# Performance work log

Measured on AMD Instinct MI355X. Metric: run time of the kernel, lower is better.

The kernel has to match this reference:

```python
import jax, jax.numpy as jnp
import numpy as np

EPS = 1e-5
L = 19        # number of semantic labels (fc_mu0..fc_mu18)
S = 512       # style_length


def conv3x3(x, w, b):
    # x: [B,C,H,W], w: [O,I,3,3] (torch OIHW), b: [O]
    y = jax.lax.conv_general_dilated(
        x, w, window_strides=(1, 1), padding='SAME',
        dimension_numbers=('NCHW', 'OIHW', 'NCHW'))
    return y + b[None, :, None, None]


def setup_inputs() -> dict:
    key = jax.random.key(0)
    ks = jax.random.split(key, 20)
    B, FIN, H, W = 4, 128, 256, 256
    inp = {
        'x': jax.random.normal(ks[0], (B, FIN, H, W), jnp.float32),
        'labels': jax.random.randint(ks[1], (B, H, W), 0, L),
        'noise': jax.random.normal(ks[2], (B, W, H, 1), jnp.float32),
        'style_codes': jax.random.normal(ks[3], (B, L, S), jnp.float32),
        # params
        'noise_var': 0.02 * jax.random.normal(ks[4], (FIN,), jnp.float32),
        'w_sh': 0.02 * jax.random.normal(ks[5], (128, L, 3, 3), jnp.float32),
        'b_sh': jnp.zeros((128,), jnp.float32),
        'w_g': 0.02 * jax.random.normal(ks[6], (FIN, 128, 3, 3), jnp.float32),
        'b_g': jnp.zeros((FIN,), jnp.float32),
        'w_b': 0.02 * jax.random.normal(ks[7], (FIN, 128, 3, 3), jnp.float32),
        'b_b': jnp.zeros((FIN,), jnp.float32),
        'Wfc': 0.02 * jax.random.normal(ks[8], (L, S, S), jnp.float32),  # [label, out, in]
        'bfc': jnp.zeros((L, S), jnp.float32),
        'w_cg': 0.02 * jax.random.normal(ks[9], (FIN, S, 3, 3), jnp.float32),
        'b_cg': jnp.zeros((FIN,), jnp.float32),
        'w_cb': 0.02 * jax.random.normal(ks[10], (FIN, S, 3, 3), jnp.float32),
        'b_cb': jnp.zeros((FIN,), jnp.float32),
        'g_blend': jnp.zeros((1,), jnp.float32),
        'b_blend': jnp.zeros((1,), jnp.float32),
    }
    return inp


def reference(x, labels, noise, style_codes, noise_var, w_sh, b_sh, w_g, b_g,
              w_b, b_b, Wfc, bfc, w_cg, b_cg, w_cb, b_cb, g_blend, b_blend):
    B, FIN, H, W = x.shape
    # added_noise: randn([B,W,H,1]) * noise_var[FIN] then transpose(1,3) -> [B,FIN,H,W]
    added = jnp.transpose(noise * noise_var, (0, 3, 2, 1))
    xn = x + added
    # param-free BatchNorm2d (training-mode batch stats, biased var)
    mean = jnp.mean(xn, axis=(0, 2, 3), keepdims=True)
    var = jnp.mean(jnp.square(xn - mean), axis=(0, 2, 3), keepdims=True)
    normalized = (xn - mean) / jnp.sqrt(var + EPS)

    # one-hot segmap [B,L,H,W]; interpolation to x's size is identity here
    seg = jnp.transpose(jax.nn.one_hot(labels, L, dtype=x.dtype), (0, 3, 1, 2))

    # per-label style FC: mu[b,j,:] = relu(fc_mu_j(style_codes[b,j]))
    mu = jax.nn.relu(jnp.einsum('bjd,jod->bjo', style_codes, Wfc) + bfc)  # [B,L,S]
    # masked_scatter with one-hot masks == per-pixel gather of the label's style code
    middle = mu[jnp.arange(B)[:, None, None], labels]        # [B,H,W,S]
    middle = jnp.transpose(middle, (0, 3, 1, 2))              # [B,S,H,W]

    gamma_avg = conv3x3(middle, w_cg, b_cg)
    beta_avg = conv3x3(middle, w_cb, b_cb)

    actv = jax.nn.relu(conv3x3(seg, w_sh, b_sh))
    gamma_spade = conv3x3(actv, w_g, b_g)
    beta_spade = conv3x3(actv, w_b, b_b)

    ga = jax.nn.sigmoid(g_blend)
    ba = jax.nn.sigmoid(b_blend)
    gamma_final = ga * gamma_avg + (1.0 - ga) * gamma_spade
    beta_final = ba * beta_avg + (1.0 - ba) * beta_spade
    return normalized * (1.0 + gamma_final) + beta_final
```

## Files before the change

### kernel.cpp

```cpp
#include <hip/hip_runtime.h>
#include <hip/hip_bf16.h>

#define NB   4
#define FIN  128
#define HH   256
#define WWW  256
#define LLAB 19
#define SSTY 512
#define HW   (HH*WWW)
#define NRED (NB*HW)

#define WS_NT   0
#define WS_SUM  262144
#define WS_SSQ  262272
#define WS_MEAN 262400
#define WS_ISTD 262528
#define WS_MU   262656
#define WS_A2   301568
#define WS_BSTG_B 1906688
#define WS_WSH_B  4855808

typedef __attribute__((ext_vector_type(8))) short bf16x8;
typedef __attribute__((ext_vector_type(4))) float f32x4;

__device__ inline unsigned short f2bf(float f) {
  __hip_bfloat16 h = __float2bfloat16(f);
  union { __hip_bfloat16 h; unsigned short u; } cv; cv.h = h; return cv.u;
}
__device__ inline float bf2f(short u) {
  union { unsigned int u; float f; } cv;
  cv.u = ((unsigned int)(unsigned short)u) << 16; return cv.f;
}

__device__ inline void gload_lds16(const void* g, void* l) {
  __builtin_amdgcn_global_load_lds(
      (const __attribute__((address_space(1))) void*)g,
      (__attribute__((address_space(3))) void*)l, 16, 0, 0);
}

__global__ __launch_bounds__(256) void k_ntrans(const float* __restrict__ noise,
                                               float* __restrict__ ws) {
  __shared__ float tile[32][33];
  const int b = blockIdx.z;
  const int w0 = blockIdx.x * 32, h0 = blockIdx.y * 32;
  const int txx = threadIdx.x, tyy = threadIdx.y;
  #pragma unroll
  for (int j = 0; j < 4; ++j) {
    int wi = w0 + tyy + j * 8;
    tile[tyy + j * 8][txx] = noise[(size_t)(b * 256 + wi) * 256 + h0 + txx];
  }
  __syncthreads();
  #pragma unroll
  for (int j = 0; j < 4; ++j) {
    int hi = h0 + tyy + j * 8;
    ws[WS_NT + (size_t)(b * 256 + hi) * 256 + w0 + txx] = tile[txx][tyy + j * 8];
  }
}

__global__ __launch_bounds__(256) void k_stats(const float* __restrict__ x,
                                               const float* __restrict__ nv,
                                               float* __restrict__ ws) {
  const int bc = blockIdx.x;
  const int b = bc >> 7, c = bc & 127;
  const int t = threadIdx.x;
  const float4* xp = (const float4*)(x + (size_t)bc * HW);
  const float4* np = (const float4*)(ws + WS_NT + (size_t)b * HW);
  const float nvc = nv[c];
  float s1 = 0.f, s2 = 0.f;
  for (int i = 0; i < 64; ++i) {
    float4 xv = xp[i * 256 + t];
    float4 nz = np[i * 256 + t];
    float v0 = xv.x + nvc * nz.x; s1 += v0; s2 = fmaf(v0, v0, s2);
    float v1 = xv.y + nvc * nz.y; s1 += v1; s2 = fmaf(v1, v1, s2);
    float v2 = xv.z + nvc * nz.z; s1 += v2; s2 = fmaf(v2, v2, s2);
    float v3 = xv.w + nvc * nz.w; s1 += v3; s2 = fmaf(v3, v3, s2);
  }
  #pragma unroll
  for (int m = 32; m; m >>= 1) { s1 += __shfl_xor(s1, m); s2 += __shfl_xor(s2, m); }
  if ((t & 63) == 0) { atomicAdd(&ws[WS_SUM + c], s1); atomicAdd(&ws[WS_SSQ + c], s2); }
}

__global__ __launch_bounds__(512) void k_mu(const float* __restrict__ style,
                                            const float* __restrict__ Wfc,
                                            const float* __restrict__ bfc,
                                            float* __restrict__ ws) {
  const int j = blockIdx.x, b = blockIdx.y, o = threadIdx.x;
  const float4* wrow = (const float4*)(Wfc + ((size_t)j * 512 + o) * 512);
  const float4* srow = (const float4*)(style + ((size_t)b * 19 + j) * 512);
  float acc = 0.f;
  for (int d = 0; d < 128; ++d) {
    float4 w = wrow[d];
    float4 s = srow[d];
    acc = fmaf(w.x, s.x, acc); acc = fmaf(w.y, s.y, acc);
    acc = fmaf(w.z, s.z, acc); acc = fmaf(w.w, s.w, acc);
  }
  acc += bfc[j * 512 + o];
  ws[WS_MU + ((size_t)b * 19 + j) * 512 + o] = fmaxf(acc, 0.f);
}

__global__ __launch_bounds__(288) void k_atab(const float* __restrict__ w_cg,
                                              const float* __restrict__ w_cb,
                                              float* __restrict__ ws) {
  __shared__ float wlds[32 * 288];
  const int t = threadIdx.x;
  const int cblk = blockIdx.x, ssplit = blockIdx.y, b = blockIdx.z;
  const int conv = t / 144, r = t % 144, cl = r / 9, k = r % 9;
  const int c = cblk * 16 + cl;
  const float* mu = ws + WS_MU;
  float acc[19];
  #pragma unroll
  for (int l = 0; l < 19; ++l) acc[l] = 0.f;

  for (int chunk = 0; chunk < 4; ++chunk) {
    const int s0 = ssplit * 128 + chunk * 32;
    for (int it = 0; it < 32; ++it) {
      int cv2 = it >> 4, cl2 = it & 15;
      const float* src = cv2 ? w_cb : w_cg;
      float v = src[((size_t)(cblk * 16 + cl2) * 512 + s0) * 9 + t];
      wlds[(t / 9) * 288 + cv2 * 144 + cl2 * 9 + (t % 9)] = v;
    }
    __syncthreads();
    for (int sl = 0; sl < 32; ++sl) {
      float w = wlds[sl * 288 + t];
      int s = s0 + sl;
      #pragma unroll
      for (int l = 0; l < 19; ++l)
        acc[l] = fmaf(mu[((size_t)b * 19 + l) * 512 + s], w, acc[l]);
    }
    __syncthreads();
  }
  #pragma unroll
  for (int l = 0; l < 19; ++l)
    atomicAdd(&ws[WS_A2 + (((size_t)b * 19 + l) * 9 + k) * 256 + conv * 128 + c], acc[l]);
}

__global__ __launch_bounds__(256) void k_pack(const float* __restrict__ w_g,
                                              const float* __restrict__ w_b,
                                              const float* __restrict__ w_sh,
                                              const float* __restrict__ g_blend,
                                              const float* __restrict__ b_blend,
                                              char* __restrict__ wsb,
                                              float* __restrict__ ws) {
  if (blockIdx.x < 144) {
    int tid = blockIdx.x * 256 + threadIdx.x;
    int lane = tid & 63, grp = tid >> 6;
    int s36 = grp % 36, nb = grp / 36;
    int kk = s36 >> 2, cb = s36 & 3;
    int n = nb * 16 + (lane & 15);
    int conv = n & 1, cout = n >> 1;
    float blend = conv ? b_blend[0] : g_blend[0];
    float scale = 1.f - 1.f / (1.f + __expf(-blend));
    const float* src = conv ? w_b : w_g;
    bf16x8 v;
    #pragma unroll
    for (int i = 0; i < 8; ++i) {
      int k = s36 * 32 + (lane >> 4) * 8 + i;
      int kki = k >> 7, cin = k & 127;
      v[i] = (short)f2bf(scale * src[((size_t)cout * 128 + cin) * 9 + kki]);
    }
    size_t slot = (size_t)(kk * 5 + cb) * 16384 + (size_t)(nb * 64 + lane) * 16;
    #pragma unroll
    for (int bb = 0; bb < 4; ++bb)
      *(bf16x8*)(wsb + WS_BSTG_B + (size_t)bb * 45 * 16384 + slot) = v;
  } else {
    int tid = (blockIdx.x - 144) * 256 + threadIdx.x;
    if (blockIdx.x == 144 && threadIdx.x < 128) {
      int c = threadIdx.x;
      float mean = ws[WS_SUM + c] / (float)NRED;
      float var = ws[WS_SSQ + c] / (float)NRED - mean * mean;
      ws[WS_MEAN + c] = mean;
      ws[WS_ISTD + c] = 1.f / sqrtf(var + 1e-5f);
    }
    if (tid < 23040) {
      int l = tid / 1152, r = tid % 1152, k = r >> 7, cin = r & 127;
      float v = (l == 0) ? 0.f : w_sh[((size_t)cin * 19 + (l - 1)) * 9 + k];
      ((unsigned short*)(wsb + WS_WSH_B))[tid] = f2bf(v);
    }
  }
}

__global__ __launch_bounds__(256) void k_packoh(const float* __restrict__ ws,
                                                const float* __restrict__ g_blend,
                                                const float* __restrict__ b_blend,
                                                char* __restrict__ wsb) {
  int tid = blockIdx.x * 256 + threadIdx.x;
  int lane = tid & 63, grp = tid >> 6;
  int kk = grp % 9, nb = (grp / 9) % 16, b = grp / 144;
  int n = nb * 16 + (lane & 15);
  int conv = n & 1, cout = n >> 1;
  float blend = conv ? b_blend[0] : g_blend[0];
  float scale = 1.f / (1.f + __expf(-blend));
  bf16x8 v;
  #pragma unroll
  for (int i = 0; i < 8; ++i) {
    int l = (lane >> 4) * 8 + i;
    float val = 0.f;
    if (l < 19)
      val = scale * ws[WS_A2 + (((size_t)b * 19 + l) * 9 + kk) * 256 + conv * 128 + cout];
    v[i] = (short)f2bf(val);
  }
  *(bf16x8*)(wsb + WS_BSTG_B + ((size_t)b * 45 + kk * 5 + 4) * 16384 +
             (size_t)(nb * 64 + lane) * 16) = v;
}

__global__ __launch_bounds__(1024, 4) void k_main(
    const float* __restrict__ x, const int* __restrict__ labels,
    const float* __restrict__ b_sh,
    const float* __restrict__ b_g, const float* __restrict__ b_b,
    const float* __restrict__ b_cg, const float* __restrict__ b_cb,
    const float* __restrict__ noise_var,
    const float* __restrict__ g_blend, const float* __restrict__ b_blend,
    const float* __restrict__ ws, float* __restrict__ out) {
  extern __shared__ char smem[];
  int* labt = (int*)smem;
  char* actv = smem + 1600;
  char* ohA  = smem + 84544;
  float* gbias = (float*)(smem + 110464);
  float* bbias = gbias + 128; float* nvl = gbias + 256;
  float* meanl = gbias + 384; float* istdl = gbias + 512; float* bshl = gbias + 640;
  char* buf0 = smem + 113536;
  char* buf1 = smem + 113536 + 16384;

  const int t = threadIdx.x;
  const int b = blockIdx.z;
  const int y0 = blockIdx.y * 16, x0 = blockIdx.x * 16;
  const char* wsb = (const char*)ws;
  const char* wshp = wsb + WS_WSH_B;

  if (t < 128) {
    float ga = 1.f / (1.f + __expf(-g_blend[0]));
    float ba = 1.f / (1.f + __expf(-b_blend[0]));
    gbias[t] = ga * b_cg[t] + (1.f - ga) * b_g[t];
    bbias[t] = ba * b_cb[t] + (1.f - ba) * b_b[t];
    nvl[t] = noise_var[t];
    meanl[t] = ws[WS_MEAN + t];
    istdl[t] = ws[WS_ISTD + t];
    bshl[t] = b_sh[t];
  }
  if (t < 400) {
    int ly = t / 20, lx = t % 20;
    int gy = y0 - 2 + ly, gx = x0 - 2 + lx;
    int v = 0;
    if ((unsigned)gy < 256u && (unsigned)gx < 256u)
      v = labels[((size_t)(b * 256 + gy)) * 256 + gx] + 1;
    labt[t] = v;
  }
  for (int i = t; i < 6480; i += 1024) ((unsigned int*)ohA)[i] = 0u;
  __syncthreads();

  for (int it = t; it < 5184; it += 1024) {
    int hp = it >> 4, cg = it & 15;
    int py = hp / 18, px = hp - py * 18;
    int gy = y0 - 1 + py, gx = x0 - 1 + px;
    int baddr = hp * 256 + ((cg * 16) ^ ((hp & 7) << 4));
    bf16x8 o = {0, 0, 0, 0, 0, 0, 0, 0};
    if ((unsigned)gy < 256u && (unsigned)gx < 256u) {
      float accv[8];
      #pragma unroll
      for (int j = 0; j < 8; ++j) accv[j] = bshl[cg * 8 + j];
      #pragma unroll
      for (int k = 0; k < 9; ++k) {
        int dy = k / 3, dx = k - 3 * (k / 3);
        int lv = labt[(py + dy) * 20 + (px + dx)];
        bf16x8 wvv = *(const bf16x8*)(wshp + (size_t)((lv * 9 + k) * 128 + cg * 8) * 2);
        #pragma unroll
        for (int j = 0; j < 8; ++j) accv[j] += bf2f(wvv[j]);
      }
      #pragma unroll
      for (int j = 0; j < 8; ++j) o[j] = (short)f2bf(fmaxf(accv[j], 0.f));
    }
    *(bf16x8*)(actv + baddr) = o;
  }
  if (t < 324) {
    int py = t / 18, px = t - (t / 18) * 18;
    int gy = y0 - 1 + py, gx = x0 - 1 + px;
    if ((unsigned)gy < 256u && (unsigned)gx < 256u) {
      int lv = labt[(py + 1) * 20 + (px + 1)];
      ((unsigned short*)ohA)[t * 40 + (lv - 1)] = 0x3F80;
    }
  }
  __syncthreads();

  const int lane = t & 63;
  const int wid = t >> 6;
  const int wm = wid & 3, wn = wid >> 2;
  const int l15 = lane & 15, l16 = lane >> 4;
  const char* bsrc = wsb + WS_BSTG_B + (size_t)b * 45 * 16384 + (size_t)t * 16;
  const int bof = (wn * 4) * 1024 + lane * 16;

  f32x4 acc[4][4];
  #pragma unroll
  for (int i = 0; i < 4; ++i)
    #pragma unroll
    for (int j = 0; j < 4; ++j) acc[i][j] = (f32x4){0.f, 0.f, 0.f, 0.f};

#define PHASE(CB, KYV, KXV, CURBUF, DO_STAGE, STG_SRC, NXTBUF, VMC) { \
  if (DO_STAGE) gload_lds16(STG_SRC, NXTBUF + t * 16); \
  asm volatile("s_waitcnt vmcnt(%0)" :: "i"(VMC) : "memory"); \
  __builtin_amdgcn_s_barrier(); \
  __builtin_amdgcn_sched_barrier(0); \
  bf16x8 bfr_[4]; \
  _Pragma("unroll") \
  for (int nf_ = 0; nf_ < 4; ++nf_) \
    bfr_[nf_] = *(const bf16x8*)(CURBUF + bof + nf_ * 1024); \
  bf16x8 af_[4]; \
  _Pragma("unroll") \
  for (int mf_ = 0; mf_ < 4; ++mf_) { \
    int hp_ = (wm * 4 + mf_ + (KYV)) * 18 + l15 + (KXV); \
    if ((CB) < 4) \
      af_[mf_] = *(const bf16x8*)(actv + hp_ * 256 + (((CB) * 64 + l16 * 16) ^ ((hp_ & 7) << 4))); \
    else \
      af_[mf_] = *(const bf16x8*)(ohA + hp_ * 80 + l16 * 16); \
  } \
  __builtin_amdgcn_s_setprio(1); \
  _Pragma("unroll") \
  for (int mf_ = 0; mf_ < 4; ++mf_) \
    _Pragma("unroll") \
    for (int nf_ = 0; nf_ < 4; ++nf_) \
      acc[mf_][nf_] = __builtin_amdgcn_mfma_f32_16x16x32_bf16(af_[mf_], bfr_[nf_], acc[mf_][nf_], 0, 0, 0); \
  __builtin_amdgcn_s_setprio(0); \
  __builtin_amdgcn_sched_barrier(0); \
  __builtin_amdgcn_s_barrier(); }

  gload_lds16(bsrc, buf0 + t * 16);

  for (int q = 0; q < 4; ++q) {
    const int kk0 = 2 * q, kk1 = kk0 + 1;
    const int ky0 = kk0 / 3, kx0 = kk0 - 3 * ky0;
    const int ky1 = kk1 / 3, kx1 = kk1 - 3 * ky1;
    const char* bq = bsrc + (size_t)q * 10 * 16384;
    PHASE(0, ky0, kx0, buf0, true, bq + 1 * 16384, buf1, 1)
    PHASE(1, ky0, kx0, buf1, true, bq + 2 * 16384, buf0, 1)
    PHASE(2, ky0, kx0, buf0, true, bq + 3 * 16384, buf1, 1)
    PHASE(3, ky0, kx0, buf1, true, bq + 4 * 16384, buf0, 1)
    PHASE(4, ky0, kx0, buf0, true, bq + 5 * 16384, buf1, 1)
    PHASE(0, ky1, kx1, buf1, true, bq + 6 * 16384, buf0, 1)
    PHASE(1, ky1, kx1, buf0, true, bq + 7 * 16384, buf1, 1)
    PHASE(2, ky1, kx1, buf1, true, bq + 8 * 16384, buf0, 1)
    PHASE(3, ky1, kx1, buf0, true, bq + 9 * 16384, buf1, 1)
    PHASE(4, ky1, kx1, buf1, true, bq + 10 * 16384, buf0, 1)
  }
  {
    const char* bq = bsrc + (size_t)40 * 16384;
    PHASE(0, 2, 2, buf0, true, bq + 1 * 16384, buf1, 1)
    PHASE(1, 2, 2, buf1, true, bq + 2 * 16384, buf0, 1)
    PHASE(2, 2, 2, buf0, true, bq + 3 * 16384, buf1, 1)
    PHASE(3, 2, 2, buf1, true, bq + 4 * 16384, buf0, 1)
    PHASE(4, 2, 2, buf0, false, bq, buf1, 0)
  }
#undef PHASE

  const float* nt = ws + WS_NT + (size_t)b * HW;
  float* eps = (float*)(smem + 1600);

  #pragma unroll
  for (int chunk = 0; chunk < 4; ++chunk) {
    __syncthreads();
    #pragma unroll
    for (int mf = 0; mf < 4; ++mf) {
      int widx = (wn * 16 + l15) * 260 + (wm * 4 + mf) * 16 + l16 * 4;
      *(f32x4*)(eps + widx) = acc[mf][chunk];
    }
    __syncthreads();
    #pragma unroll
    for (int rep = 0; rep < 2; ++rep) {
      int u = rep * 1024 + t;
      int xq = u & 3, y = (u >> 2) & 15, ci = u >> 6;
      int wnp = ci >> 3, q = ci & 7;
      int c = wnp * 32 + chunk * 8 + q;
      int rg = wnp * 16 + 2 * q;
      f32x4 g4 = *(const f32x4*)(eps + rg * 260 + y * 16 + xq * 4);
      f32x4 b4 = *(const f32x4*)(eps + (rg + 1) * 260 + y * 16 + xq * 4);
      const float gb_ = gbias[c], bb_ = bbias[c];
      const float mn = meanl[c], is = istdl[c], nv = nvl[c];
      size_t off = (((size_t)(b * 128 + c)) * 256 + (y0 + y)) * 256 + x0 + xq * 4;
      float4 xv = *(const float4*)(x + off);
      float4 nz = *(const float4*)(nt + (y0 + y) * 256 + x0 + xq * 4);
      float4 o;
      o.x = ((xv.x + nv * nz.x) - mn) * is * (1.f + g4[0] + gb_) + (b4[0] + bb_);
      o.y = ((xv.y + nv * nz.y) - mn) * is * (1.f + g4[1] + gb_) + (b4[1] + bb_);
      o.z = ((xv.z + nv * nz.z) - mn) * is * (1.f + g4[2] + gb_) + (b4[2] + bb_);
      o.w = ((xv.w + nv * nz.w) - mn) * is * (1.f + g4[3] + gb_) + (b4[3] + bb_);
      *(float4*)(out + off) = o;
    }
  }
}

extern "C" void kernel_launch(void* const* d_in, const int* in_sizes, int n_in,
                              void* d_out, int out_size, void* d_ws, size_t ws_size,
                              hipStream_t stream) {
  const float* x        = (const float*)d_in[0];
  const int*   labels   = (const int*)d_in[1];
  const float* noise    = (const float*)d_in[2];
  const float* style    = (const float*)d_in[3];
  const float* nvar     = (const float*)d_in[4];
  const float* w_sh     = (const float*)d_in[5];
  const float* b_sh     = (const float*)d_in[6];
  const float* w_g      = (const float*)d_in[7];
  const float* b_g      = (const float*)d_in[8];
  const float* w_b      = (const float*)d_in[9];
  const float* b_b      = (const float*)d_in[10];
  const float* Wfc      = (const float*)d_in[11];
  const float* bfc      = (const float*)d_in[12];
  const float* w_cg     = (const float*)d_in[13];
  const float* b_cg     = (const float*)d_in[14];
  const float* w_cb     = (const float*)d_in[15];
  const float* b_cb     = (const float*)d_in[16];
  const float* g_blend  = (const float*)d_in[17];
  const float* b_blend  = (const float*)d_in[18];
  float* ws  = (float*)d_ws;
  char*  wsb = (char*)d_ws;
  float* out = (float*)d_out;

  static bool attr_set = false;
  if (!attr_set) {
    (void)hipFuncSetAttribute((const void*)k_main,
                              hipFuncAttributeMaxDynamicSharedMemorySize, 146304);
    attr_set = true;
  }

  hipMemsetAsync((char*)d_ws + (size_t)WS_SUM * 4, 0, 256 * 4, stream);
  hipMemsetAsync((char*)d_ws + (size_t)WS_A2 * 4, 0, (size_t)175104 * 4, stream);

  k_ntrans<<<dim3(8, 8, 4), dim3(32, 8), 0, stream>>>(noise, ws);
  k_stats<<<dim3(512), dim3(256), 0, stream>>>(x, nvar, ws);
  k_mu<<<dim3(19, 4), dim3(512), 0, stream>>>(style, Wfc, bfc, ws);
  k_atab<<<dim3(8, 4, 4), dim3(288), 0, stream>>>(w_cg, w_cb, ws);
  k_pack<<<dim3(234), dim3(256), 0, stream>>>(w_g, w_b, w_sh, g_blend, b_blend, wsb, ws);
  k_packoh<<<dim3(144), dim3(256), 0, stream>>>(ws, g_blend, b_blend, wsb);
  k_main<<<dim3(16, 16, 4), dim3(1024), 146304, stream>>>(
      x, labels, b_sh, b_g, b_b, b_cg, b_cb,
      nvar, g_blend, b_blend, ws, out);
}
```

Before: 320.0 us.

## Merge six prep kernels into three by block-index dispatch, widen LDS swizzle

The six small preprocessing kernels become three launches. Independent stages (noise transpose with the style FC, BN stats with the A-table contraction, weight packing with the one-hot pack) now share a grid and are picked by block index. This removes launch gaps and lets independent work overlap, at the cost of heterogeneous blocks and a 512-thread shape for the stats path. Separately, the activation LDS swizzle XOR now uses 4 bits of the row index instead of 3, to cut bank conflicts on A-fragment reads in the main MFMA kernel.

```diff
diff --git a/kernel.cpp b/kernel.cpp
--- a/kernel.cpp
+++ b/kernel.cpp
@@ -38,103 +38,112 @@
       (__attribute__((address_space(3))) void*)l, 16, 0, 0);
 }
 
-__global__ __launch_bounds__(256) void k_ntrans(const float* __restrict__ noise,
-                                               float* __restrict__ ws) {
-  __shared__ float tile[32][33];
-  const int b = blockIdx.z;
-  const int w0 = blockIdx.x * 32, h0 = blockIdx.y * 32;
-  const int txx = threadIdx.x, tyy = threadIdx.y;
-  #pragma unroll
-  for (int j = 0; j < 4; ++j) {
-    int wi = w0 + tyy + j * 8;
-    tile[tyy + j * 8][txx] = noise[(size_t)(b * 256 + wi) * 256 + h0 + txx];
-  }
-  __syncthreads();
-  #pragma unroll
-  for (int j = 0; j < 4; ++j) {
-    int hi = h0 + tyy + j * 8;
-    ws[WS_NT + (size_t)(b * 256 + hi) * 256 + w0 + txx] = tile[txx][tyy + j * 8];
-  }
-}
-
-__global__ __launch_bounds__(256) void k_stats(const float* __restrict__ x,
-                                               const float* __restrict__ nv,
-                                               float* __restrict__ ws) {
-  const int bc = blockIdx.x;
-  const int b = bc >> 7, c = bc & 127;
+__global__ __launch_bounds__(256) void kprep1(const float* __restrict__ noise,
+                                              const float* __restrict__ style,
+                                              const float* __restrict__ Wfc,
+                                              const float* __restrict__ bfc,
+                                              float* __restrict__ ws) {
   const int t = threadIdx.x;
-  const float4* xp = (const float4*)(x + (size_t)bc * HW);
-  const float4* np = (const float4*)(ws + WS_NT + (size_t)b * HW);
-  const float nvc = nv[c];
-  float s1 = 0.f, s2 = 0.f;
-  for (int i = 0; i < 64; ++i) {
-    float4 xv = xp[i * 256 + t];
-    float4 nz = np[i * 256 + t];
-    float v0 = xv.x + nvc * nz.x; s1 += v0; s2 = fmaf(v0, v0, s2);
-    float v1 = xv.y + nvc * nz.y; s1 += v1; s2 = fmaf(v1, v1, s2);
-    float v2 = xv.z + nvc * nz.z; s1 += v2; s2 = fmaf(v2, v2, s2);
-    float v3 = xv.w + nvc * nz.w; s1 += v3; s2 = fmaf(v3, v3, s2);
-  }
-  #pragma unroll
-  for (int m = 32; m; m >>= 1) { s1 += __shfl_xor(s1, m); s2 += __shfl_xor(s2, m); }
-  if ((t & 63) == 0) { atomicAdd(&ws[WS_SUM + c], s1); atomicAdd(&ws[WS_SSQ + c], s2); }
-}
-
-__global__ __launch_bounds__(512) void k_mu(const float* __restrict__ style,
-                                            const float* __restrict__ Wfc,
-                                            const float* __restrict__ bfc,
-                                            float* __restrict__ ws) {
-  const int j = blockIdx.x, b = blockIdx.y, o = threadIdx.x;
-  const float4* wrow = (const float4*)(Wfc + ((size_t)j * 512 + o) * 512);
-  const float4* srow = (const float4*)(style + ((size_t)b * 19 + j) * 512);
-  float acc = 0.f;
-  for (int d = 0; d < 128; ++d) {
-    float4 w = wrow[d];
-    float4 s = srow[d];
-    acc = fmaf(w.x, s.x, acc); acc = fmaf(w.y, s.y, acc);
-    acc = fmaf(w.z, s.z, acc); acc = fmaf(w.w, s.w, acc);
-  }
-  acc += bfc[j * 512 + o];
-  ws[WS_MU + ((size_t)b * 19 + j) * 512 + o] = fmaxf(acc, 0.f);
-}
-
-__global__ __launch_bounds__(288) void k_atab(const float* __restrict__ w_cg,
+  if (blockIdx.x < 256) {
+    __shared__ float tile[32][33];
+    int blk = blockIdx.x;
+    int b = blk >> 6, by = (blk >> 3) & 7, bx = blk & 7;
+    int w0 = bx * 32, h0 = by * 32;
+    int txx = t & 31, tyy = t >> 5;
+    #pragma unroll
+    for (int j = 0; j < 4; ++j) {
+      int wi = w0 + tyy + j * 8;
+      tile[tyy + j * 8][txx] = noise[(size_t)(b * 256 + wi) * 256 + h0 + txx];
+    }
+    __syncthreads();
+    #pragma unroll
+    for (int j = 0; j < 4; ++j) {
+      int hi = h0 + tyy + j * 8;
+      ws[WS_NT + (size_t)(b * 256 + hi) * 256 + w0 + txx] = tile[txx][tyy + j * 8];
+    }
+  } else {
+    int m = blockIdx.x - 256;
+    int j = m >> 3, r = m & 7, b = r >> 1, half = r & 1;
+    int o = half * 256 + t;
+    const float4* wrow = (const float4*)(Wfc + ((size_t)j * 512 + o) * 512);
+    const float4* srow = (const float4*)(style + ((size_t)b * 19 + j) * 512);
+    float acc = 0.f;
+    for (int d = 0; d < 128; ++d) {
+      float4 w = wrow[d];
+      float4 s = srow[d];
+      acc = fmaf(w.x, s.x, acc); acc = fmaf(w.y, s.y, acc);
+      acc = fmaf(w.z, s.z, acc); acc = fmaf(w.w, s.w, acc);
+    }
+    acc += bfc[j * 512 + o];
+    ws[WS_MU + ((size_t)b * 19 + j) * 512 + o] = fmaxf(acc, 0.f);
+  }
+}
+
+__global__ __launch_bounds__(512) void kprep2(const float* __restrict__ x,
+                                              const float* __restrict__ nv,
+                                              const float* __restrict__ w_cg,
                                               const float* __restrict__ w_cb,
                                               float* __restrict__ ws) {
-  __shared__ float wlds[32 * 288];
   const int t = threadIdx.x;
-  const int cblk = blockIdx.x, ssplit = blockIdx.y, b = blockIdx.z;
-  const int conv = t / 144, r = t % 144, cl = r / 9, k = r % 9;
-  const int c = cblk * 16 + cl;
-  const float* mu = ws + WS_MU;
-  float acc[19];
-  #pragma unroll
-  for (int l = 0; l < 19; ++l) acc[l] = 0.f;
-
-  for (int chunk = 0; chunk < 4; ++chunk) {
-    const int s0 = ssplit * 128 + chunk * 32;
-    for (int it = 0; it < 32; ++it) {
-      int cv2 = it >> 4, cl2 = it & 15;
-      const float* src = cv2 ? w_cb : w_cg;
-      float v = src[((size_t)(cblk * 16 + cl2) * 512 + s0) * 9 + t];
-      wlds[(t / 9) * 288 + cv2 * 144 + cl2 * 9 + (t % 9)] = v;
-    }
-    __syncthreads();
-    for (int sl = 0; sl < 32; ++sl) {
-      float w = wlds[sl * 288 + t];
-      int s = s0 + sl;
+  if (blockIdx.x < 512) {
+    const int bc = blockIdx.x;
+    const int b = bc >> 7, c = bc & 127;
+    const float4* xp = (const float4*)(x + (size_t)bc * HW);
+    const float4* np = (const float4*)(ws + WS_NT + (size_t)b * HW);
+    const float nvc = nv[c];
+    float s1 = 0.f, s2 = 0.f;
+    for (int i = 0; i < 32; ++i) {
+      float4 xv = xp[i * 512 + t];
+      float4 nz = np[i * 512 + t];
+      float v0 = xv.x + nvc * nz.x; s1 += v0; s2 = fmaf(v0, v0, s2);
+      float v1 = xv.y + nvc * nz.y; s1 += v1; s2 = fmaf(v1, v1, s2);
+      float v2 = xv.z + nvc * nz.z; s1 += v2; s2 = fmaf(v2, v2, s2);
+      float v3 = xv.w + nvc * nz.w; s1 += v3; s2 = fmaf(v3, v3, s2);
+    }
+    #pragma unroll
+    for (int m = 32; m; m >>= 1) { s1 += __shfl_xor(s1, m); s2 += __shfl_xor(s2, m); }
+    if ((t & 63) == 0) { atomicAdd(&ws[WS_SUM + c], s1); atomicAdd(&ws[WS_SSQ + c], s2); }
+  } else {
+    __shared__ float wlds[32 * 288];
+    const int blkm = blockIdx.x - 512;
+    const int cblk = blkm & 7, ssplit = (blkm >> 3) & 3, b = blkm >> 5;
+    const int conv = t / 144, r = t % 144, cl = r / 9, k = r % 9;
+    const int c = cblk * 16 + cl;
+    const float* mu = ws + WS_MU;
+    float acc[19];
+    #pragma unroll
+    for (int l = 0; l < 19; ++l) acc[l] = 0.f;
+
+    for (int chunk = 0; chunk < 4; ++chunk) {
+      const int s0 = ssplit * 128 + chunk * 32;
+      for (int i = t; i < 9216; i += 512) {
+        int kx = i % 9, q = i / 9, sl = q & 31, cc = q >> 5;
+        int cv2 = cc >> 4, cl2 = cc & 15;
+        const float* src = cv2 ? w_cb : w_cg;
+        float v = src[((size_t)(cblk * 16 + cl2) * 512 + s0 + sl) * 9 + kx];
+        wlds[sl * 288 + cv2 * 144 + cl2 * 9 + kx] = v;
+      }
+      __syncthreads();
+      if (t < 288) {
+        for (int sl = 0; sl < 32; ++sl) {
+          float w = wlds[sl * 288 + t];
+          int s = s0 + sl;
+          #pragma unroll
+          for (int l = 0; l < 19; ++l)
+            acc[l] = fmaf(mu[((size_t)b * 19 + l) * 512 + s], w, acc[l]);
+        }
+      }
+      __syncthreads();
+    }
+    if (t < 288) {
       #pragma unroll
       for (int l = 0; l < 19; ++l)
-        acc[l] = fmaf(mu[((size_t)b * 19 + l) * 512 + s], w, acc[l]);
-    }
-    __syncthreads();
-  }
-  #pragma unroll
-  for (int l = 0; l < 19; ++l)
-    atomicAdd(&ws[WS_A2 + (((size_t)b * 19 + l) * 9 + k) * 256 + conv * 128 + c], acc[l]);
-}
-
-__global__ __launch_bounds__(256) void k_pack(const float* __restrict__ w_g,
+        atomicAdd(&ws[WS_A2 + (((size_t)b * 19 + l) * 9 + k) * 256 + conv * 128 + c], acc[l]);
+    }
+  }
+}
+
+__global__ __launch_bounds__(256) void kprep3(const float* __restrict__ w_g,
                                               const float* __restrict__ w_b,
                                               const float* __restrict__ w_sh,
                                               const float* __restrict__ g_blend,
@@ -162,7 +171,7 @@
     #pragma unroll
     for (int bb = 0; bb < 4; ++bb)
       *(bf16x8*)(wsb + WS_BSTG_B + (size_t)bb * 45 * 16384 + slot) = v;
-  } else {
+  } else if (blockIdx.x < 234) {
     int tid = (blockIdx.x - 144) * 256 + threadIdx.x;
     if (blockIdx.x == 144 && threadIdx.x < 128) {
       int c = threadIdx.x;
@@ -176,31 +185,26 @@
       float v = (l == 0) ? 0.f : w_sh[((size_t)cin * 19 + (l - 1)) * 9 + k];
       ((unsigned short*)(wsb + WS_WSH_B))[tid] = f2bf(v);
     }
-  }
-}
-
-__global__ __launch_bounds__(256) void k_packoh(const float* __restrict__ ws,
-                                                const float* __restrict__ g_blend,
-                                                const float* __restrict__ b_blend,
-                                                char* __restrict__ wsb) {
-  int tid = blockIdx.x * 256 + threadIdx.x;
-  int lane = tid & 63, grp = tid >> 6;
-  int kk = grp % 9, nb = (grp / 9) % 16, b = grp / 144;
-  int n = nb * 16 + (lane & 15);
-  int conv = n & 1, cout = n >> 1;
-  float blend = conv ? b_blend[0] : g_blend[0];
-  float scale = 1.f / (1.f + __expf(-blend));
-  bf16x8 v;
-  #pragma unroll
-  for (int i = 0; i < 8; ++i) {
-    int l = (lane >> 4) * 8 + i;
-    float val = 0.f;
-    if (l < 19)
-      val = scale * ws[WS_A2 + (((size_t)b * 19 + l) * 9 + kk) * 256 + conv * 128 + cout];
-    v[i] = (short)f2bf(val);
-  }
-  *(bf16x8*)(wsb + WS_BSTG_B + ((size_t)b * 45 + kk * 5 + 4) * 16384 +
-             (size_t)(nb * 64 + lane) * 16) = v;
+  } else {
+    int tid = (blockIdx.x - 234) * 256 + threadIdx.x;
+    int lane = tid & 63, grp = tid >> 6;
+    int kk = grp % 9, nb = (grp / 9) % 16, b = grp / 144;
+    int n = nb * 16 + (lane & 15);
+    int conv = n & 1, cout = n >> 1;
+    float blend = conv ? b_blend[0] : g_blend[0];
+    float scale = 1.f / (1.f + __expf(-blend));
+    bf16x8 v;
+    #pragma unroll
+    for (int i = 0; i < 8; ++i) {
+      int l = (lane >> 4) * 8 + i;
+      float val = 0.f;
+      if (l < 19)
+        val = scale * ws[WS_A2 + (((size_t)b * 19 + l) * 9 + kk) * 256 + conv * 128 + cout];
+      v[i] = (short)f2bf(val);
+    }
+    *(bf16x8*)(wsb + WS_BSTG_B + ((size_t)b * 45 + kk * 5 + 4) * 16384 +
+               (size_t)(nb * 64 + lane) * 16) = v;
+  }
 }
 
 __global__ __launch_bounds__(1024, 4) void k_main(
@@ -252,7 +256,7 @@
     int hp = it >> 4, cg = it & 15;
     int py = hp / 18, px = hp - py * 18;
     int gy = y0 - 1 + py, gx = x0 - 1 + px;
-    int baddr = hp * 256 + ((cg * 16) ^ ((hp & 7) << 4));
+    int baddr = hp * 256 + ((cg * 16) ^ ((hp & 15) << 4));
     bf16x8 o = {0, 0, 0, 0, 0, 0, 0, 0};
     if ((unsigned)gy < 256u && (unsigned)gx < 256u) {
       float accv[8];
@@ -308,7 +312,7 @@
   for (int mf_ = 0; mf_ < 4; ++mf_) { \
     int hp_ = (wm * 4 + mf_ + (KYV)) * 18 + l15 + (KXV); \
     if ((CB) < 4) \
-      af_[mf_] = *(const bf16x8*)(actv + hp_ * 256 + (((CB) * 64 + l16 * 16) ^ ((hp_ & 7) << 4))); \
+      af_[mf_] = *(const bf16x8*)(actv + hp_ * 256 + (((CB) * 64 + l16 * 16) ^ ((hp_ & 15) << 4))); \
     else \
       af_[mf_] = *(const bf16x8*)(ohA + hp_ * 80 + l16 * 16); \
   } \
@@ -422,12 +426,9 @@
   hipMemsetAsync((char*)d_ws + (size_t)WS_SUM * 4, 0, 256 * 4, stream);
   hipMemsetAsync((char*)d_ws + (size_t)WS_A2 * 4, 0, (size_t)175104 * 4, stream);
 
-  k_ntrans<<<dim3(8, 8, 4), dim3(32, 8), 0, stream>>>(noise, ws);
-  k_stats<<<dim3(512), dim3(256), 0, stream>>>(x, nvar, ws);
-  k_mu<<<dim3(19, 4), dim3(512), 0, stream>>>(style, Wfc, bfc, ws);
-  k_atab<<<dim3(8, 4, 4), dim3(288), 0, stream>>>(w_cg, w_cb, ws);
-  k_pack<<<dim3(234), dim3(256), 0, stream>>>(w_g, w_b, w_sh, g_blend, b_blend, wsb, ws);
-  k_packoh<<<dim3(144), dim3(256), 0, stream>>>(ws, g_blend, b_blend, wsb);
+  kprep1<<<dim3(408), dim3(256), 0, stream>>>(noise, style, Wfc, bfc, ws);
+  kprep2<<<dim3(640), dim3(512), 0, stream>>>(x, nvar, w_cg, w_cb, ws);
+  kprep3<<<dim3(378), dim3(256), 0, stream>>>(w_g, w_b, w_sh, g_blend, b_blend, wsb, ws);
   k_main<<<dim3(16, 16, 4), dim3(1024), 146304, stream>>>(
       x, labels, b_sh, b_g, b_b, b_cg, b_cb,
       nvar, g_blend, b_blend, ws, out);
```

Measured after the change: 303.2 us. 1.06x faster.
